# Performance work log

Hardware: AMD Instinct MI355X
Metric: run time of the kernel (lower is better)

The kernel has to match this reference:

```python
import jax, jax.numpy as jnp
import numpy as np

NUM_CODES = 100000
DIM = 64
N_VISITS = 16384
MAX_CODES = 64


def setup_inputs() -> dict:
    key = jax.random.key(0)
    k1, k2 = jax.random.split(key)
    # ids in [-5, NUM_CODES): negatives act as padding (original filters ids >= 0)
    code_ids = jax.random.randint(k1, (N_VISITS, MAX_CODES), -5, NUM_CODES, dtype=jnp.int64)
    emb_weight = jax.random.normal(k2, (NUM_CODES, DIM), dtype=jnp.float32)
    return {"code_ids": code_ids, "emb_weight": emb_weight}


def reference(code_ids, emb_weight):
    # mask of valid (non-negative) code ids per visit
    mask = code_ids >= 0                                  # [N, C] bool
    safe_ids = jnp.where(mask, code_ids, 0)               # clamp padding to 0 for gather
    x = emb_weight[safe_ids]                              # [N, C, D] gather
    maskf = mask.astype(emb_weight.dtype)
    sums = jnp.einsum('ncd,nc->nd', x, maskf)             # masked sum over codes
    counts = maskf.sum(axis=1, keepdims=True)             # [N, 1]
    # mean over valid ids; visits with zero valid ids -> zero vector
    out = sums / jnp.maximum(counts, 1.0)
    return jnp.where(counts > 0, out, 0.0)
```

## Files before the change

kernel.cpp:

```cpp
#include <hip/hip_runtime.h>

#define N_VISITS  16384
#define MAX_CODES 64
#define DIM       64

__global__ __launch_bounds__(256) void visit_mean_kernel(
    const int* __restrict__ code_ids,
    const float* __restrict__ emb,
    float* __restrict__ out)
{
    const int wave_in_block = threadIdx.x >> 6;
    const int lane = threadIdx.x & 63;
    const int visit = blockIdx.x * 4 + wave_in_block;

    const int r = lane >> 4;
    const int t = lane & 15;

    const int my_id = code_ids[(size_t)visit * MAX_CODES + lane];
    const unsigned long long valid = __ballot(my_id >= 0);
    const int count = __popcll(valid);

    int ids[16];
    #pragma unroll
    for (int j = 0; j < 16; ++j) {
        ids[j] = __shfl(my_id, 4 * j + r, 64);
    }

    float4 v[16];
    #pragma unroll
    for (int j = 0; j < 16; ++j) {
        const int id   = ids[j];
        const int safe = (id >= 0) ? id : 0;
        v[j] = *((const float4*)(emb + (size_t)safe * DIM) + t);
    }

    float4 acc = make_float4(0.f, 0.f, 0.f, 0.f);
    #pragma unroll
    for (int j = 0; j < 16; ++j) {
        const float m = (ids[j] >= 0) ? 1.0f : 0.0f;
        acc.x = fmaf(m, v[j].x, acc.x);
        acc.y = fmaf(m, v[j].y, acc.y);
        acc.z = fmaf(m, v[j].z, acc.z);
        acc.w = fmaf(m, v[j].w, acc.w);
    }

    acc.x += __shfl_xor(acc.x, 16, 64);
    acc.y += __shfl_xor(acc.y, 16, 64);
    acc.z += __shfl_xor(acc.z, 16, 64);
    acc.w += __shfl_xor(acc.w, 16, 64);
    acc.x += __shfl_xor(acc.x, 32, 64);
    acc.y += __shfl_xor(acc.y, 32, 64);
    acc.z += __shfl_xor(acc.z, 32, 64);
    acc.w += __shfl_xor(acc.w, 32, 64);

    if (lane < 16) {
        const float scale = (count > 0) ? (1.0f / (float)count) : 0.0f;
        float4 o;
        o.x = acc.x * scale;
        o.y = acc.y * scale;
        o.z = acc.z * scale;
        o.w = acc.w * scale;
        ((float4*)(out + (size_t)visit * DIM))[t] = o;
    }
}

extern "C" void kernel_launch(void* const* d_in, const int* in_sizes, int n_in,
                              void* d_out, int out_size, void* d_ws, size_t ws_size,
                              hipStream_t stream) {
    const int*   code_ids = (const int*)d_in[0];
    const float* emb      = (const float*)d_in[1];
    float*       out      = (float*)d_out;

    const int waves_per_block = 4;
    const int grid = N_VISITS / waves_per_block;
    visit_mean_kernel<<<grid, 256, 0, stream>>>(code_ids, emb, out);
}
```

Measured before the change: 99.55 us.

## Convert embedding table to fp16 in workspace before gather-mean

Adds a pre-pass kernel that converts the fp32 embedding table to fp16 in the workspace on every call. The gather kernel then reads half-precision rows, with 8 lanes per row instead of 16, and accumulates in fp32. This halves the bytes per gathered row, at the cost of an extra full-table read and write each call and fp16 rounding of the embeddings. Nontemporal loads and stores are also used for the ids and the output.

```diff
diff --git a/kernel.cpp b/kernel.cpp
--- a/kernel.cpp
+++ b/kernel.cpp
@@ -1,66 +1,93 @@
 #include <hip/hip_runtime.h>
+#include <hip/hip_fp16.h>
 
 #define N_VISITS  16384
 #define MAX_CODES 64
 #define DIM       64
+#define NUM_CODES 100000
+
+typedef float f32x4 __attribute__((ext_vector_type(4)));
+
+__global__ __launch_bounds__(256) void emb_to_half_kernel(
+    const float* __restrict__ emb, __half* __restrict__ embh)
+{
+    const size_t n8 = (size_t)NUM_CODES * DIM / 8;
+    size_t i = (size_t)blockIdx.x * blockDim.x + threadIdx.x;
+    const size_t stride = (size_t)gridDim.x * blockDim.x;
+    for (; i < n8; i += stride) {
+        const f32x4* src = (const f32x4*)emb + 2 * i;
+        f32x4 a = __builtin_nontemporal_load(src);
+        f32x4 b = __builtin_nontemporal_load(src + 1);
+        union { __half2 h[4]; f32x4 f; } u;
+        u.h[0] = __floats2half2_rn(a.x, a.y);
+        u.h[1] = __floats2half2_rn(a.z, a.w);
+        u.h[2] = __floats2half2_rn(b.x, b.y);
+        u.h[3] = __floats2half2_rn(b.z, b.w);
+        ((f32x4*)embh)[i] = u.f;
+    }
+}
 
 __global__ __launch_bounds__(256) void visit_mean_kernel(
     const int* __restrict__ code_ids,
-    const float* __restrict__ emb,
+    const __half* __restrict__ embh,
     float* __restrict__ out)
 {
     const int wave_in_block = threadIdx.x >> 6;
     const int lane = threadIdx.x & 63;
     const int visit = blockIdx.x * 4 + wave_in_block;
 
-    const int r = lane >> 4;
-    const int t = lane & 15;
+    const int r = lane >> 3;
+    const int t = lane & 7;
 
-    const int my_id = code_ids[(size_t)visit * MAX_CODES + lane];
+    const int my_id = __builtin_nontemporal_load(
+        code_ids + (size_t)visit * MAX_CODES + lane);
     const unsigned long long valid = __ballot(my_id >= 0);
     const int count = __popcll(valid);
 
-    int ids[16];
+    int ids[8];
     #pragma unroll
-    for (int j = 0; j < 16; ++j) {
-        ids[j] = __shfl(my_id, 4 * j + r, 64);
+    for (int j = 0; j < 8; ++j) {
+        ids[j] = __shfl(my_id, 8 * j + r, 64);
     }
 
-    float4 v[16];
+    f32x4 v[8];
     #pragma unroll
-    for (int j = 0; j < 16; ++j) {
+    for (int j = 0; j < 8; ++j) {
         const int id   = ids[j];
         const int safe = (id >= 0) ? id : 0;
-        v[j] = *((const float4*)(emb + (size_t)safe * DIM) + t);
+        v[j] = *((const f32x4*)(embh + (size_t)safe * DIM) + t);
     }
 
-    float4 acc = make_float4(0.f, 0.f, 0.f, 0.f);
+    float acc[8] = {0.f, 0.f, 0.f, 0.f, 0.f, 0.f, 0.f, 0.f};
     #pragma unroll
-    for (int j = 0; j < 16; ++j) {
+    for (int j = 0; j < 8; ++j) {
         const float m = (ids[j] >= 0) ? 1.0f : 0.0f;
-        acc.x = fmaf(m, v[j].x, acc.x);
-        acc.y = fmaf(m, v[j].y, acc.y);
-        acc.z = fmaf(m, v[j].z, acc.z);
-        acc.w = fmaf(m, v[j].w, acc.w);
+        const __half2* h = (const __half2*)&v[j];
+        #pragma unroll
+        for (int k = 0; k < 4; ++k) {
+            const float2 f = __half22float2(h[k]);
+            acc[2 * k]     = fmaf(m, f.x, acc[2 * k]);
+            acc[2 * k + 1] = fmaf(m, f.y, acc[2 * k + 1]);
+        }
     }
 
-    acc.x += __shfl_xor(acc.x, 16, 64);
-    acc.y += __shfl_xor(acc.y, 16, 64);
-    acc.z += __shfl_xor(acc.z, 16, 64);
-    acc.w += __shfl_xor(acc.w, 16, 64);
-    acc.x += __shfl_xor(acc.x, 32, 64);
-    acc.y += __shfl_xor(acc.y, 32, 64);
-    acc.z += __shfl_xor(acc.z, 32, 64);
-    acc.w += __shfl_xor(acc.w, 32, 64);
+    #pragma unroll
+    for (int k = 0; k < 8; ++k) acc[k] += __shfl_xor(acc[k], 8, 64);
+    #pragma unroll
+    for (int k = 0; k < 8; ++k) acc[k] += __shfl_xor(acc[k], 16, 64);
+    #pragma unroll
+    for (int k = 0; k < 8; ++k) acc[k] += __shfl_xor(acc[k], 32, 64);
 
-    if (lane < 16) {
+    if (lane < 8) {
         const float scale = (count > 0) ? (1.0f / (float)count) : 0.0f;
-        float4 o;
-        o.x = acc.x * scale;
-        o.y = acc.y * scale;
-        o.z = acc.z * scale;
-        o.w = acc.w * scale;
-        ((float4*)(out + (size_t)visit * DIM))[t] = o;
+        f32x4 o0, o1;
+        o0.x = acc[0] * scale; o0.y = acc[1] * scale;
+        o0.z = acc[2] * scale; o0.w = acc[3] * scale;
+        o1.x = acc[4] * scale; o1.y = acc[5] * scale;
+        o1.z = acc[6] * scale; o1.w = acc[7] * scale;
+        f32x4* dst = (f32x4*)(out + (size_t)visit * DIM + lane * 8);
+        __builtin_nontemporal_store(o0, dst);
+        __builtin_nontemporal_store(o1, dst + 1);
     }
 }
 
@@ -70,8 +97,11 @@
     const int*   code_ids = (const int*)d_in[0];
     const float* emb      = (const float*)d_in[1];
     float*       out      = (float*)d_out;
+    __half*      embh     = (__half*)d_ws;
+
+    emb_to_half_kernel<<<2048, 256, 0, stream>>>(emb, embh);
 
     const int waves_per_block = 4;
     const int grid = N_VISITS / waves_per_block;
-    visit_mean_kernel<<<grid, 256, 0, stream>>>(code_ids, emb, out);
+    visit_mean_kernel<<<grid, 256, 0, stream>>>(code_ids, embh, out);
 }
```

Result: faster. 94.11 us (-5.5%).
